# Optimization experiments

Measured on AMD Instinct MI355X. Metric: run time of the kernel, lower is better.

## Reference

```python
import jax, jax.numpy as jnp
import numpy as np

EPS = 1e-5

def conv1x1(x, W, b):
    # x: [B,C,H,W], W: [O,C], b: [O] -- a 1x1 conv is a per-pixel matmul
    return jnp.einsum('bchw,oc->bohw', x, W) + b[None, :, None, None]

def mean_variance_norm(feat):
    # torch .var(dim=2) is unbiased (ddof=1)
    m = feat.mean(axis=(2, 3), keepdims=True)
    v = feat.var(axis=(2, 3), ddof=1, keepdims=True)
    return (feat - m) / jnp.sqrt(v + EPS)

def setup_inputs() -> dict:
    key = jax.random.key(0)
    ks = jax.random.split(key, 10)
    B, C, H, W = 4, 256, 64, 64
    sc = 1.0 / np.sqrt(C)
    return {
        'content': jax.random.normal(ks[0], (B, C, H, W), jnp.float32),
        'style': jax.random.normal(ks[1], (B, C, H, W), jnp.float32),
        'content_key': jax.random.normal(ks[2], (B, C, H, W), jnp.float32),
        'style_key': jax.random.normal(ks[3], (B, C, H, W), jnp.float32),
        'Wf': jax.random.normal(ks[4], (C, C), jnp.float32) * sc,
        'bf': jnp.zeros((C,), jnp.float32),
        'Wg': jax.random.normal(ks[5], (C, C), jnp.float32) * sc,
        'bg': jnp.zeros((C,), jnp.float32),
        'Wh': jax.random.normal(ks[6], (C, C), jnp.float32) * sc,
        'bh': jnp.zeros((C,), jnp.float32),
    }

def reference(content, style, content_key, style_key, Wf, bf, Wg, bg, Wh, bh):
    Fq = conv1x1(content_key, Wf, bf)   # [B,Ck,H,W]
    G = conv1x1(style_key, Wg, bg)      # [B,Ck,Hs,Ws]
    Hv = conv1x1(style, Wh, bh)         # [B,C,Hs,Ws]
    b, _, h, w = Fq.shape
    _, C, hs, ws = Hv.shape
    N, M = h * w, hs * ws
    q = Fq.reshape(b, -1, N).transpose(0, 2, 1)   # [B,N,Ck]
    k = G.reshape(b, -1, M)                        # [B,Ck,M]
    style_flat = Hv.reshape(b, C, M).transpose(0, 2, 1)  # [B,M,C]
    # masks are all-ones -> attn_mask all zeros -> no masking (faithful to None path)
    S = jax.nn.softmax(jnp.einsum('bnc,bcm->bnm', q, k), axis=-1)  # [B,N,M]
    mean = jnp.einsum('bnm,bmc->bnc', S, style_flat)               # [B,N,C]
    std = jnp.sqrt(jax.nn.relu(
        jnp.einsum('bnm,bmc->bnc', S, style_flat * style_flat) - mean * mean))
    mean = mean.reshape(b, h, w, C).transpose(0, 3, 1, 2)  # [B,C,H,W]
    std = std.reshape(b, h, w, C).transpose(0, 3, 1, 2)
    return std * mean_variance_norm(content) + mean
```

## Files before the change

kernel.cpp:

```cpp
#include <hip/hip_runtime.h>


typedef unsigned int u32;
typedef unsigned short u16;
typedef _Float16 f16x8 __attribute__((ext_vector_type(8)));
typedef float f32x4 __attribute__((ext_vector_type(4)));
typedef float f32x16 __attribute__((ext_vector_type(16)));
typedef unsigned int u32x2 __attribute__((ext_vector_type(2)));
typedef unsigned __attribute__((address_space(3))) as3_u32;
typedef const unsigned __attribute__((address_space(1))) as1_u32;

#define L2E 1.44269504088896340736f
#define MFMA(a, b, c) __builtin_amdgcn_mfma_f32_16x16x32_f16(a, b, c, 0, 0, 0)
#define MFMA32(a, b, c) __builtin_amdgcn_mfma_f32_32x32x16_f16(a, b, c, 0, 0, 0)
#define EXP2(x) __builtin_amdgcn_exp2f(x)

__device__ __forceinline__ u16 h_bits(_Float16 h) { return __builtin_bit_cast(u16, h); }
__device__ __forceinline__ u16 f2h(float f) { return h_bits((_Float16)f); }
__device__ __forceinline__ u32 pk2(float a, float b) {
    return (u32)f2h(a) | ((u32)f2h(b) << 16);
}

__device__ __forceinline__ f16x8 ldh8(const u16* p) {
    uint4 v = *(const uint4*)p;
    return __builtin_bit_cast(f16x8, v);
}

__device__ __forceinline__ void gll16(const u16* g, const void* lds) {
    __builtin_amdgcn_global_load_lds((as1_u32*)g,
                                     (as3_u32*)(unsigned)(unsigned long long)lds,
                                     16, 0, 0);
}

__device__ __forceinline__ u32x2 pl32_swap(u32 a, u32 b) {
#if __has_builtin(__builtin_amdgcn_permlane32_swap)
    return __builtin_amdgcn_permlane32_swap(a, b, false, false);
#else
    asm("v_permlane32_swap_b32 %0, %1" : "+v"(a), "+v"(b));
    u32x2 r; r.x = a; r.y = b; return r;
#endif
}

__global__ void k_stats(const float* __restrict__ content,
                        float* __restrict__ cm, float* __restrict__ cr) {
    int blk = blockIdx.x;
    const float* p = content + (size_t)blk * 4096;
    int t = threadIdx.x;
    float s = 0.f, ss = 0.f;
    for (int i = 0; i < 4; i++) {
        float4 v = *(const float4*)(p + (i * 256 + t) * 4);
        s  += (v.x + v.y) + (v.z + v.w);
        ss += (v.x * v.x + v.y * v.y) + (v.z * v.z + v.w * v.w);
    }
    for (int d = 32; d >= 1; d >>= 1) { s += __shfl_xor(s, d); ss += __shfl_xor(ss, d); }
    __shared__ __align__(16) float as[4], ass[4];
    int w = t >> 6;
    if ((t & 63) == 0) { as[w] = s; ass[w] = ss; }
    __syncthreads();
    if (t == 0) {
        s  = (as[0] + as[1]) + (as[2] + as[3]);
        ss = (ass[0] + ass[1]) + (ass[2] + ass[3]);
        float mean = s * (1.0f / 4096.0f);
        float var = (ss - s * mean) * (1.0f / 4095.0f);
        cm[blk] = mean;
        cr[blk] = rsqrtf(var + 1e-5f);
    }
}

__global__ void k_prep(const float* __restrict__ style, const float* __restrict__ ckey,
                       const float* __restrict__ skey,
                       const float* __restrict__ Wf, const float* __restrict__ Wg,
                       const float* __restrict__ Wh,
                       u16* __restrict__ X1, u16* __restrict__ X2, u16* __restrict__ Cc,
                       u16* __restrict__ Wb) {
    int z = blockIdx.z, t = threadIdx.x;
    if (z >= 12) {
        if (blockIdx.y != 0) return;
        int m = z - 12;
        const float* src = (m == 0) ? Wf : ((m == 1) ? Wg : Wh);
        u16* dst = Wb + m * 65536;
        int i = (blockIdx.x * 256 + t) * 4;
        float4 v = *(const float4*)(src + i);
        ushort4 o;
        o.x = f2h(v.x); o.y = f2h(v.y); o.z = f2h(v.z); o.w = f2h(v.w);
        *(ushort4*)(dst + i) = o;
        return;
    }
    int tensor = z >> 2, b = z & 3;
    const float* src = ((tensor == 0) ? style : ((tensor == 1) ? ckey : skey))
                       + (size_t)b * 256 * 4096;
    u16* dst = ((tensor == 0) ? X1 : ((tensor == 1) ? X2 : Cc)) + (size_t)b * 4096 * 256;
    int c0 = blockIdx.y * 64, t0 = blockIdx.x * 64;
    __shared__ __align__(16) float ls[64][65];
    int tr = t >> 4, tc = t & 15;
    for (int i = 0; i < 4; i++) {
        int c_off = i * 16 + tr;
        float4 v = *(const float4*)(src + (size_t)(c0 + c_off) * 4096 + t0 + tc * 4);
        ls[tc * 4 + 0][c_off] = v.x;
        ls[tc * 4 + 1][c_off] = v.y;
        ls[tc * 4 + 2][c_off] = v.z;
        ls[tc * 4 + 3][c_off] = v.w;
    }
    __syncthreads();
    for (int i = 0; i < 4; i++) {
        int tokrow = i * 16 + tr;
        ushort4 o;
        o.x = f2h(ls[tokrow][tc * 4 + 0]);
        o.y = f2h(ls[tokrow][tc * 4 + 1]);
        o.z = f2h(ls[tokrow][tc * 4 + 2]);
        o.w = f2h(ls[tokrow][tc * 4 + 3]);
        *(ushort4*)(dst + (size_t)(t0 + tokrow) * 256 + c0 + tc * 4) = o;
    }
}

__launch_bounds__(256, 2)
__global__ void k_gemm(const u16* X1, const u16* X2, u16* Cc,
                       u16* A, u16* Bv, const u16* __restrict__ Wb,
                       const float* __restrict__ bfp, const float* __restrict__ bgp,
                       const float* __restrict__ bhp) {
    int mode = blockIdx.z, b = blockIdx.y, tok0 = blockIdx.x * 128;
    const u16* X = ((mode == 0) ? X2 : ((mode == 1) ? (const u16*)Cc : X1))
                   + (size_t)b * 4096 * 256;
    const u16* W = Wb + mode * 65536;
    const float* bias = (mode == 0) ? bfp : ((mode == 1) ? bgp : bhp);
    __shared__ __align__(16) u16 wt[256 * 40];
    int t = threadIdx.x, w = t >> 6, lane = t & 63, ln = lane & 15, quad = lane >> 4;

    f32x4 acc[8][4];
    for (int i = 0; i < 8; i++)
        for (int j = 0; j < 4; j++) acc[i][j] = f32x4{0.f, 0.f, 0.f, 0.f};

    for (int ks = 0; ks < 8; ks++) {
        {
            const u16* wr = W + t * 256 + ks * 32;
            uint4 w0 = *(const uint4*)(wr + 0);
            uint4 w1 = *(const uint4*)(wr + 8);
            uint4 w2 = *(const uint4*)(wr + 16);
            uint4 w3 = *(const uint4*)(wr + 24);
            *(uint4*)(wt + t * 40 + 0)  = w0;
            *(uint4*)(wt + t * 40 + 8)  = w1;
            *(uint4*)(wt + t * 40 + 16) = w2;
            *(uint4*)(wt + t * 40 + 24) = w3;
        }
        __syncthreads();
        f16x8 wf[4];
        #pragma unroll
        for (int ct = 0; ct < 4; ct++)
            wf[ct] = ldh8(wt + (w * 64 + ct * 16 + ln) * 40 + quad * 8);
        #pragma unroll
        for (int rt = 0; rt < 8; rt++) {
            f16x8 xf = ldh8(X + (size_t)(tok0 + rt * 16 + ln) * 256 + ks * 32 + quad * 8);
            if (mode < 2) {
                #pragma unroll
                for (int ct = 0; ct < 4; ct++) acc[rt][ct] = MFMA(xf, wf[ct], acc[rt][ct]);
            } else {
                #pragma unroll
                for (int ct = 0; ct < 4; ct++) acc[rt][ct] = MFMA(wf[ct], xf, acc[rt][ct]);
            }
        }
        __syncthreads();
    }

    if (mode < 2) {
        u16* O = ((mode == 0) ? A : Cc) + (size_t)b * 4096 * 256;
        float bv[4];
        #pragma unroll
        for (int ct = 0; ct < 4; ct++) bv[ct] = bias[w * 64 + ct * 16 + ln];
        #pragma unroll
        for (int rt = 0; rt < 8; rt++)
            #pragma unroll
            for (int ct = 0; ct < 4; ct++)
                #pragma unroll
                for (int r = 0; r < 4; r++) {
                    int tok = tok0 + rt * 16 + quad * 4 + r;
                    int o = w * 64 + ct * 16 + ln;
                    O[(size_t)tok * 256 + o] = f2h(acc[rt][ct][r] + bv[ct]);
                }
    } else {
        u16* OV = Bv + (size_t)b * 256 * 4096;
        #pragma unroll
        for (int ct = 0; ct < 4; ct++)
            #pragma unroll
            for (int r = 0; r < 4; r++) {
                int o = w * 64 + ct * 16 + quad * 4 + r;
                float bb = bias[o];
                #pragma unroll
                for (int rt = 0; rt < 8; rt++) {
                    int tok = tok0 + rt * 16 + ln;
                    OV[(size_t)o * 4096 + tok] = f2h(acc[rt][ct][r] + bb);
                }
            }
    }
}

__launch_bounds__(256)
__attribute__((amdgpu_waves_per_eu(2, 2)))
__global__ void k_flash(const u16* __restrict__ Qt, const u16* __restrict__ Kt,
                        const u16* __restrict__ Vt,
                        const float* __restrict__ content, const float* __restrict__ cm,
                        const float* __restrict__ cr, float* __restrict__ out) {
    __shared__ __align__(16) char smem[67584];
    const u16* KsU = (const u16*)smem;
    int t = threadIdx.x, w = t >> 6, l = t & 63, lq = l & 31, h = l >> 5;

    int b = blockIdx.y, q0 = blockIdx.x * 128, coff = blockIdx.z * 64;

    const u16* Kg = Kt + (size_t)b * 4096 * 256;
    const u16* Vg = Vt + ((size_t)b * 256 + coff) * 4096;

    const u16* ksrc;
    {
        int qb = w * 1024 + l * 16;
        int r0 = qb >> 9;
        int swz = (qb & 511) ^ ((r0 & 7) << 4);
        ksrc = Kg + r0 * 256 + (swz >> 1);
    }
    const char* ldsKw = smem + w * 1024;

    int uu = (h ^ (lq & 7)) << 3;
    int tab0 = uu, tab1 = 16 ^ uu, tab2 = 32 ^ uu, tab3 = 48 ^ uu;
    int kb0 = lq * 256;

    f16x8 qf[16];
    {
        const u16* qp = Qt + ((size_t)b * 4096 + q0 + w * 32 + lq) * 256 + h * 8;
        #pragma unroll
        for (int ks = 0; ks < 16; ks++) qf[ks] = ldh8(qp + ks * 16);
    }

    f32x16 am[2], aq[2];
    #pragma unroll
    for (int i = 0; i < 16; i++) { am[0][i] = 0.f; am[1][i] = 0.f; aq[0][i] = 0.f; aq[1][i] = 0.f; }
    float mrow = -1e30f, lrow = 0.f;

    #pragma unroll
    for (int i = 0; i < 8; i++) gll16(ksrc + i * 2048, ldsKw + i * 4096);
    asm volatile("s_waitcnt vmcnt(0)" ::: "memory");
    __builtin_amdgcn_s_barrier();

    int koffB = 0;
    for (int it = 0; it < 64; it++) {
        if (it < 63) {
            int m0n = (it + 1) * 16384;
            #pragma unroll
            for (int i = 0; i < 8; i++)
                gll16(ksrc + m0n + i * 2048, ldsKw + (koffB ^ 32768) + i * 4096);
        }

        int kb = (koffB >> 1) + kb0;
        f32x16 s0, s1;
        #pragma unroll
        for (int i = 0; i < 16; i++) { s0[i] = 0.f; s1[i] = 0.f; }
        __builtin_amdgcn_s_setprio(1);
        #pragma unroll
        for (int ks = 0; ks < 16; ks++) {
            int off = ((ks & 3) == 0 ? tab0 : (ks & 3) == 1 ? tab1
                      : (ks & 3) == 2 ? tab2 : tab3) + (ks >> 2) * 64;
            f16x8 k0 = ldh8(KsU + kb + off);
            s0 = MFMA32(k0, qf[ks], s0);
            f16x8 k1 = ldh8(KsU + kb + 8192 + off);
            s1 = MFMA32(k1, qf[ks], s1);
        }
        __builtin_amdgcn_s_setprio(0);

        const u16* Vit = Vg + it * 64;
        f16x8 vfr[4][2];
        #pragma unroll
        for (int ks = 0; ks < 4; ks++)
            #pragma unroll
            for (int ct = 0; ct < 2; ct++)
                vfr[ks][ct] = ldh8(Vit + (size_t)(ct * 32 + lq) * 4096 + ks * 16 + h * 8);

        float m8[8];
        #pragma unroll
        for (int r = 0; r < 8; r++)
            m8[r] = fmaxf(fmaxf(s0[r], s0[r + 8]), fmaxf(s1[r], s1[r + 8]));
        #pragma unroll
        for (int d = 4; d >= 1; d >>= 1)
            #pragma unroll
            for (int r = 0; r < d; r++) m8[r] = fmaxf(m8[r], m8[r + d]);
        float mt = fmaxf(m8[0], __shfl_xor(m8[0], 32));

        float mn, al;
        bool resc = !__all(mt - mrow <= 8.0f);
        if (resc) {
            mn = fmaxf(mrow, mt);
            al = EXP2((mrow - mn) * L2E);
            mrow = mn;
        } else {
            mn = mrow;
            al = 1.0f;
        }
        float base = mn * L2E;
        #pragma unroll
        for (int r = 0; r < 16; r++) {
            float p0 = (float)(_Float16)EXP2(__builtin_fmaf(s0[r], L2E, -base));
            float p1 = (float)(_Float16)EXP2(__builtin_fmaf(s1[r], L2E, -base));
            s0[r] = p0; s1[r] = p1;
        }
        float a8[8];
        #pragma unroll
        for (int r = 0; r < 8; r++)
            a8[r] = (s0[r] + s0[r + 8]) + (s1[r] + s1[r + 8]);
        #pragma unroll
        for (int d = 4; d >= 1; d >>= 1)
            #pragma unroll
            for (int r = 0; r < d; r++) a8[r] += a8[r + d];
        float rs = a8[0] + __shfl_xor(a8[0], 32);
        lrow = lrow * al + rs;

        if (resc) {
            #pragma unroll
            for (int r = 0; r < 16; r++) {
                float sc = __shfl(al, 8 * (r >> 2) + 4 * h + (r & 3));
                am[0][r] *= sc; am[1][r] *= sc;
                aq[0][r] *= sc; aq[1][r] *= sc;
            }
        }

        f16x8 pfr[4];
        #pragma unroll
        for (int mt2 = 0; mt2 < 2; mt2++) {
            f32x16 sv = mt2 ? s1 : s0;
            u32 d0 = pk2(sv[0], sv[1]),  d1 = pk2(sv[2], sv[3]);
            u32 d2 = pk2(sv[4], sv[5]),  d3 = pk2(sv[6], sv[7]);
            u32 d4 = pk2(sv[8], sv[9]),  d5 = pk2(sv[10], sv[11]);
            u32 d6 = pk2(sv[12], sv[13]), d7 = pk2(sv[14], sv[15]);
            u32x2 p02 = pl32_swap(d0, d2);
            u32x2 p13 = pl32_swap(d1, d3);
            u32x2 p46 = pl32_swap(d4, d6);
            u32x2 p57 = pl32_swap(d5, d7);
            uint4 fa = {p02.x, p13.x, p02.y, p13.y};
            uint4 fb = {p46.x, p57.x, p46.y, p57.y};
            pfr[mt2 * 2 + 0] = __builtin_bit_cast(f16x8, fa);
            pfr[mt2 * 2 + 1] = __builtin_bit_cast(f16x8, fb);
        }

        __builtin_amdgcn_s_setprio(1);
        #pragma unroll
        for (int ks = 0; ks < 4; ks++) {
            f16x8 pf = pfr[ks];
            #pragma unroll
            for (int ct = 0; ct < 2; ct++) {
                f16x8 vf = vfr[ks][ct];
                am[ct] = MFMA32(pf, vf, am[ct]);
                f16x8 vh = vf * vf;
                f16x8 vl = __builtin_elementwise_fma(vf, vf, -vh);
                aq[ct] = MFMA32(pf, vh, aq[ct]);
                aq[ct] = MFMA32(pf, vl, aq[ct]);
            }
        }
        __builtin_amdgcn_s_setprio(0);

        asm volatile("s_waitcnt vmcnt(0)" ::: "memory");
        __builtin_amdgcn_s_barrier();
        koffB ^= 32768;
    }

    float inv = 1.0f / lrow;
    float iv[16];
    #pragma unroll
    for (int r = 0; r < 16; r++) iv[r] = __shfl(inv, (r & 3) + 8 * (r >> 2) + 4 * h);
    float* Ms = (float*)smem;
    float* Ss = (float*)(smem + 33792);
    #pragma unroll
    for (int ct = 0; ct < 2; ct++)
        #pragma unroll
        for (int rq = 0; rq < 4; rq++) {
            f32x4 mv, sv;
            #pragma unroll
            for (int j = 0; j < 4; j++) {
                int r = 4 * rq + j;
                float mean = am[ct][r] * iv[r];
                float ex2 = aq[ct][r] * iv[r];
                float var = ex2 - mean * mean;
                mv[j] = mean;
                sv[j] = sqrtf(fmaxf(var, 0.f));
            }
            int c = ct * 32 + lq;
            int qloc = w * 32 + 8 * rq + 4 * h;
            *(f32x4*)(Ms + c * 132 + qloc) = mv;
            *(f32x4*)(Ss + c * 132 + qloc) = sv;
        }
    __syncthreads();
    #pragma unroll
    for (int pass = 0; pass < 8; pass++) {
        int c = pass * 8 + (t >> 5);
        int qloc = (t & 31) * 4;
        f32x4 mv = *(const f32x4*)(Ms + c * 132 + qloc);
        f32x4 sv = *(const f32x4*)(Ss + c * 132 + qloc);
        int gc = coff + c;
        size_t basei = ((size_t)b * 256 + gc) * 4096 + q0 + qloc;
        float4 cv = *(const float4*)(content + basei);
        float cmv = cm[b * 256 + gc], crv = cr[b * 256 + gc];
        float4 o;
        o.x = sv[0] * ((cv.x - cmv) * crv) + mv[0];
        o.y = sv[1] * ((cv.y - cmv) * crv) + mv[1];
        o.z = sv[2] * ((cv.z - cmv) * crv) + mv[2];
        o.w = sv[3] * ((cv.w - cmv) * crv) + mv[3];
        *(float4*)(out + basei) = o;
    }
}

extern "C" void kernel_launch(void* const* d_in, const int* in_sizes, int n_in,
                              void* d_out, int out_size, void* d_ws, size_t ws_size,
                              hipStream_t stream) {
    const float* content = (const float*)d_in[0];
    const float* style   = (const float*)d_in[1];
    const float* ckey    = (const float*)d_in[2];
    const float* skey    = (const float*)d_in[3];
    const float* Wf      = (const float*)d_in[4];
    const float* bfp     = (const float*)d_in[5];
    const float* Wg      = (const float*)d_in[6];
    const float* bgp     = (const float*)d_in[7];
    const float* Wh      = (const float*)d_in[8];
    const float* bhp     = (const float*)d_in[9];
    float* out = (float*)d_out;
    char* ws = (char*)d_ws;

    float* cm = (float*)(ws + 0);
    float* cr = (float*)(ws + 4096);
    u16*   Wb = (u16*)(ws + 8192);
    u16*   A  = (u16*)(ws + 1048576);
    u16*   Bv = (u16*)(ws + 9437184);
    u16*   Cc = (u16*)(ws + 17825792);
    u16*   X1 = (u16*)d_out;
    u16*   X2 = (u16*)d_out + 4194304;

    k_stats<<<dim3(1024), 256, 0, stream>>>(content, cm, cr);
    k_prep<<<dim3(64, 4, 15), 256, 0, stream>>>(style, ckey, skey, Wf, Wg, Wh,
                                                X1, X2, Cc, Wb);
    k_gemm<<<dim3(32, 4, 3), 256, 0, stream>>>(X1, X2, Cc, A, Bv, Wb, bfp, bgp, bhp);
    k_flash<<<dim3(32, 4, 4), 256, 0, stream>>>(A, Cc, Bv, content, cm, cr, out);
}
```

Baseline: 406.8 us.

## Defer PV MFMAs by one iteration to overlap with softmax

The P·V and P·V² MFMA accumulation is software-pipelined: each iteration keeps its packed probabilities and V fragments in registers, and issues them at the start of the next iteration, alongside the max/sum reductions. A drain step after the loop finishes the last tile. This lets the matrix unit run while the softmax VALU work executes, instead of running serially after it. In exchange, V loads are now waited on at the end-of-iteration vmcnt(0), so they no longer hide behind the QK MFMAs. Register pressure also rises from the held fragments, and the setprio hints around PV are dropped.

```diff
diff --git a/kernel.cpp b/kernel.cpp
--- a/kernel.cpp
+++ b/kernel.cpp
@@ -233,6 +233,15 @@
     for (int i = 0; i < 16; i++) { am[0][i] = 0.f; am[1][i] = 0.f; aq[0][i] = 0.f; aq[1][i] = 0.f; }
     float mrow = -1e30f, lrow = 0.f;
 
+    f16x8 pheld[4];
+    f16x8 vheld[4][2];
+    #pragma unroll
+    for (int i = 0; i < 4; i++) {
+        pheld[i] = f16x8{0, 0, 0, 0, 0, 0, 0, 0};
+        vheld[i][0] = f16x8{0, 0, 0, 0, 0, 0, 0, 0};
+        vheld[i][1] = f16x8{0, 0, 0, 0, 0, 0, 0, 0};
+    }
+
     #pragma unroll
     for (int i = 0; i < 8; i++) gll16(ksrc + i * 2048, ldsKw + i * 4096);
     asm volatile("s_waitcnt vmcnt(0)" ::: "memory");
@@ -263,13 +272,19 @@
         }
         __builtin_amdgcn_s_setprio(0);
 
-        const u16* Vit = Vg + it * 64;
-        f16x8 vfr[4][2];
-        #pragma unroll
-        for (int ks = 0; ks < 4; ks++)
-            #pragma unroll
-            for (int ct = 0; ct < 2; ct++)
-                vfr[ks][ct] = ldh8(Vit + (size_t)(ct * 32 + lq) * 4096 + ks * 16 + h * 8);
+        #pragma unroll
+        for (int ks = 0; ks < 4; ks++) {
+            f16x8 pf = pheld[ks];
+            #pragma unroll
+            for (int ct = 0; ct < 2; ct++) {
+                f16x8 vf = vheld[ks][ct];
+                am[ct] = MFMA32(pf, vf, am[ct]);
+                f16x8 vh = vf * vf;
+                f16x8 vl = __builtin_elementwise_fma(vf, vf, -vh);
+                aq[ct] = MFMA32(pf, vh, aq[ct]);
+                aq[ct] = MFMA32(pf, vl, aq[ct]);
+            }
+        }
 
         float m8[8];
         #pragma unroll
@@ -318,7 +333,6 @@
             }
         }
 
-        f16x8 pfr[4];
         #pragma unroll
         for (int mt2 = 0; mt2 < 2; mt2++) {
             f32x16 sv = mt2 ? s1 : s0;
@@ -332,29 +346,37 @@
             u32x2 p57 = pl32_swap(d5, d7);
             uint4 fa = {p02.x, p13.x, p02.y, p13.y};
             uint4 fb = {p46.x, p57.x, p46.y, p57.y};
-            pfr[mt2 * 2 + 0] = __builtin_bit_cast(f16x8, fa);
-            pfr[mt2 * 2 + 1] = __builtin_bit_cast(f16x8, fb);
-        }
-
-        __builtin_amdgcn_s_setprio(1);
-        #pragma unroll
-        for (int ks = 0; ks < 4; ks++) {
-            f16x8 pf = pfr[ks];
-            #pragma unroll
-            for (int ct = 0; ct < 2; ct++) {
-                f16x8 vf = vfr[ks][ct];
-                am[ct] = MFMA32(pf, vf, am[ct]);
-                f16x8 vh = vf * vf;
-                f16x8 vl = __builtin_elementwise_fma(vf, vf, -vh);
-                aq[ct] = MFMA32(pf, vh, aq[ct]);
-                aq[ct] = MFMA32(pf, vl, aq[ct]);
-            }
-        }
-        __builtin_amdgcn_s_setprio(0);
+            pheld[mt2 * 2 + 0] = __builtin_bit_cast(f16x8, fa);
+            pheld[mt2 * 2 + 1] = __builtin_bit_cast(f16x8, fb);
+        }
+
+        {
+            const u16* Vit = Vg + it * 64;
+            #pragma unroll
+            for (int ks = 0; ks < 4; ks++)
+                #pragma unroll
+                for (int ct = 0; ct < 2; ct++)
+                    vheld[ks][ct] =
+                        ldh8(Vit + (size_t)(ct * 32 + lq) * 4096 + ks * 16 + h * 8);
+        }
 
         asm volatile("s_waitcnt vmcnt(0)" ::: "memory");
         __builtin_amdgcn_s_barrier();
         koffB ^= 32768;
+    }
+
+    #pragma unroll
+    for (int ks = 0; ks < 4; ks++) {
+        f16x8 pf = pheld[ks];
+        #pragma unroll
+        for (int ct = 0; ct < 2; ct++) {
+            f16x8 vf = vheld[ks][ct];
+            am[ct] = MFMA32(pf, vf, am[ct]);
+            f16x8 vh = vf * vf;
+            f16x8 vl = __builtin_elementwise_fma(vf, vf, -vh);
+            aq[ct] = MFMA32(pf, vh, aq[ct]);
+            aq[ct] = MFMA32(pf, vl, aq[ct]);
+        }
     }
 
     float inv = 1.0f / lrow;
```

Result: slower. 419.5 us (+3.1%).

## Split KV tile across wave pairs in flash kernel and merge softmax partials

Applied to the files above, without the earlier changes.

The flash kernel now handles 64 queries per block instead of 128, with the four waves arranged as two query groups times two key halves. Each wave runs its own online softmax over half of every 64-key tile, and the two halves are merged through LDS at the end. The double-buffered K prefetch is replaced by a single buffer that is loaded at the top of each iteration and waited on before use. LDS use drops and the grid doubles, with waves_per_eu raised to 3 so more blocks can be resident, at the cost of exposed K load latency, extra barriers and a final reduction step.

```diff
diff --git a/kernel.cpp b/kernel.cpp
--- a/kernel.cpp
+++ b/kernel.cpp
@@ -194,36 +194,37 @@
 }
 
 __launch_bounds__(256)
-__attribute__((amdgpu_waves_per_eu(2, 2)))
+__attribute__((amdgpu_waves_per_eu(3)))
 __global__ void k_flash(const u16* __restrict__ Qt, const u16* __restrict__ Kt,
                         const u16* __restrict__ Vt,
                         const float* __restrict__ content, const float* __restrict__ cm,
                         const float* __restrict__ cr, float* __restrict__ out) {
-    __shared__ __align__(16) char smem[67584];
+    __shared__ __align__(16) char smem[36864];
     const u16* KsU = (const u16*)smem;
-    int t = threadIdx.x, w = t >> 6, l = t & 63, lq = l & 31, h = l >> 5;
-
-    int b = blockIdx.y, q0 = blockIdx.x * 128, coff = blockIdx.z * 64;
+    int t = threadIdx.x, w4 = t >> 6, l = t & 63, lq = l & 31, h = l >> 5;
+    int qg = w4 & 1, mh = w4 >> 1;
+
+    int b = blockIdx.y, q0 = blockIdx.x * 64, coff = blockIdx.z * 64;
 
     const u16* Kg = Kt + (size_t)b * 4096 * 256;
-    const u16* Vg = Vt + ((size_t)b * 256 + coff) * 4096;
+    const u16* Vg = Vt + ((size_t)b * 256 + coff) * 4096 + mh * 32;
 
     const u16* ksrc;
     {
-        int qb = w * 1024 + l * 16;
+        int qb = w4 * 1024 + l * 16;
         int r0 = qb >> 9;
         int swz = (qb & 511) ^ ((r0 & 7) << 4);
         ksrc = Kg + r0 * 256 + (swz >> 1);
     }
-    const char* ldsKw = smem + w * 1024;
+    const char* ldsKw = smem + w4 * 1024;
 
     int uu = (h ^ (lq & 7)) << 3;
     int tab0 = uu, tab1 = 16 ^ uu, tab2 = 32 ^ uu, tab3 = 48 ^ uu;
-    int kb0 = lq * 256;
+    int kb0 = (mh * 32 + lq) * 256;
 
     f16x8 qf[16];
     {
-        const u16* qp = Qt + ((size_t)b * 4096 + q0 + w * 32 + lq) * 256 + h * 8;
+        const u16* qp = Qt + ((size_t)b * 4096 + q0 + qg * 32 + lq) * 256 + h * 8;
         #pragma unroll
         for (int ks = 0; ks < 16; ks++) qf[ks] = ldh8(qp + ks * 16);
     }
@@ -233,48 +234,51 @@
     for (int i = 0; i < 16; i++) { am[0][i] = 0.f; am[1][i] = 0.f; aq[0][i] = 0.f; aq[1][i] = 0.f; }
     float mrow = -1e30f, lrow = 0.f;
 
-    #pragma unroll
-    for (int i = 0; i < 8; i++) gll16(ksrc + i * 2048, ldsKw + i * 4096);
-    asm volatile("s_waitcnt vmcnt(0)" ::: "memory");
-    __builtin_amdgcn_s_barrier();
-
-    int koffB = 0;
     for (int it = 0; it < 64; it++) {
-        if (it < 63) {
-            int m0n = (it + 1) * 16384;
+        {
+            int m0 = it * 16384;
             #pragma unroll
             for (int i = 0; i < 8; i++)
-                gll16(ksrc + m0n + i * 2048, ldsKw + (koffB ^ 32768) + i * 4096);
-        }
-
-        int kb = (koffB >> 1) + kb0;
-        f32x16 s0, s1;
-        #pragma unroll
-        for (int i = 0; i < 16; i++) { s0[i] = 0.f; s1[i] = 0.f; }
+                gll16(ksrc + m0 + i * 2048, ldsKw + i * 4096);
+        }
+        asm volatile("" ::: "memory");
+        f16x8 vfr[2][2];
+        {
+            const u16* Vit = Vg + it * 64;
+            #pragma unroll
+            for (int ks = 0; ks < 2; ks++)
+                #pragma unroll
+                for (int ct = 0; ct < 2; ct++)
+                    vfr[ks][ct] = ldh8(Vit + (size_t)(ct * 32 + lq) * 4096 + ks * 16 + h * 8);
+        }
+        asm volatile("s_waitcnt vmcnt(4)" ::: "memory");
+        __builtin_amdgcn_s_barrier();
+        asm volatile("" ::: "memory");
+
+        f32x16 sA, sB;
+        #pragma unroll
+        for (int i = 0; i < 16; i++) { sA[i] = 0.f; sB[i] = 0.f; }
         __builtin_amdgcn_s_setprio(1);
         #pragma unroll
-        for (int ks = 0; ks < 16; ks++) {
+        for (int ks = 0; ks < 8; ks++) {
             int off = ((ks & 3) == 0 ? tab0 : (ks & 3) == 1 ? tab1
                       : (ks & 3) == 2 ? tab2 : tab3) + (ks >> 2) * 64;
-            f16x8 k0 = ldh8(KsU + kb + off);
-            s0 = MFMA32(k0, qf[ks], s0);
-            f16x8 k1 = ldh8(KsU + kb + 8192 + off);
-            s1 = MFMA32(k1, qf[ks], s1);
+            sA = MFMA32(ldh8(KsU + kb0 + off), qf[ks], sA);
+        }
+        #pragma unroll
+        for (int ks = 8; ks < 16; ks++) {
+            int off = ((ks & 3) == 0 ? tab0 : (ks & 3) == 1 ? tab1
+                      : (ks & 3) == 2 ? tab2 : tab3) + (ks >> 2) * 64;
+            sB = MFMA32(ldh8(KsU + kb0 + off), qf[ks], sB);
         }
         __builtin_amdgcn_s_setprio(0);
-
-        const u16* Vit = Vg + it * 64;
-        f16x8 vfr[4][2];
-        #pragma unroll
-        for (int ks = 0; ks < 4; ks++)
-            #pragma unroll
-            for (int ct = 0; ct < 2; ct++)
-                vfr[ks][ct] = ldh8(Vit + (size_t)(ct * 32 + lq) * 4096 + ks * 16 + h * 8);
+        f32x16 s;
+        #pragma unroll
+        for (int i = 0; i < 16; i++) s[i] = sA[i] + sB[i];
 
         float m8[8];
         #pragma unroll
-        for (int r = 0; r < 8; r++)
-            m8[r] = fmaxf(fmaxf(s0[r], s0[r + 8]), fmaxf(s1[r], s1[r + 8]));
+        for (int r = 0; r < 8; r++) m8[r] = fmaxf(s[r], s[r + 8]);
         #pragma unroll
         for (int d = 4; d >= 1; d >>= 1)
             #pragma unroll
@@ -293,15 +297,11 @@
         }
         float base = mn * L2E;
         #pragma unroll
-        for (int r = 0; r < 16; r++) {
-            float p0 = (float)(_Float16)EXP2(__builtin_fmaf(s0[r], L2E, -base));
-            float p1 = (float)(_Float16)EXP2(__builtin_fmaf(s1[r], L2E, -base));
-            s0[r] = p0; s1[r] = p1;
-        }
+        for (int r = 0; r < 16; r++)
+            s[r] = (float)(_Float16)EXP2(__builtin_fmaf(s[r], L2E, -base));
         float a8[8];
         #pragma unroll
-        for (int r = 0; r < 8; r++)
-            a8[r] = (s0[r] + s0[r + 8]) + (s1[r] + s1[r + 8]);
+        for (int r = 0; r < 8; r++) a8[r] = s[r] + s[r + 8];
         #pragma unroll
         for (int d = 4; d >= 1; d >>= 1)
             #pragma unroll
@@ -318,27 +318,25 @@
             }
         }
 
-        f16x8 pfr[4];
-        #pragma unroll
-        for (int mt2 = 0; mt2 < 2; mt2++) {
-            f32x16 sv = mt2 ? s1 : s0;
-            u32 d0 = pk2(sv[0], sv[1]),  d1 = pk2(sv[2], sv[3]);
-            u32 d2 = pk2(sv[4], sv[5]),  d3 = pk2(sv[6], sv[7]);
-            u32 d4 = pk2(sv[8], sv[9]),  d5 = pk2(sv[10], sv[11]);
-            u32 d6 = pk2(sv[12], sv[13]), d7 = pk2(sv[14], sv[15]);
+        f16x8 pfr[2];
+        {
+            u32 d0 = pk2(s[0], s[1]),   d1 = pk2(s[2], s[3]);
+            u32 d2 = pk2(s[4], s[5]),   d3 = pk2(s[6], s[7]);
+            u32 d4 = pk2(s[8], s[9]),   d5 = pk2(s[10], s[11]);
+            u32 d6 = pk2(s[12], s[13]), d7 = pk2(s[14], s[15]);
             u32x2 p02 = pl32_swap(d0, d2);
             u32x2 p13 = pl32_swap(d1, d3);
             u32x2 p46 = pl32_swap(d4, d6);
             u32x2 p57 = pl32_swap(d5, d7);
             uint4 fa = {p02.x, p13.x, p02.y, p13.y};
             uint4 fb = {p46.x, p57.x, p46.y, p57.y};
-            pfr[mt2 * 2 + 0] = __builtin_bit_cast(f16x8, fa);
-            pfr[mt2 * 2 + 1] = __builtin_bit_cast(f16x8, fb);
+            pfr[0] = __builtin_bit_cast(f16x8, fa);
+            pfr[1] = __builtin_bit_cast(f16x8, fb);
         }
 
         __builtin_amdgcn_s_setprio(1);
         #pragma unroll
-        for (int ks = 0; ks < 4; ks++) {
+        for (int ks = 0; ks < 2; ks++) {
             f16x8 pf = pfr[ks];
             #pragma unroll
             for (int ct = 0; ct < 2; ct++) {
@@ -352,43 +350,98 @@
         }
         __builtin_amdgcn_s_setprio(0);
 
-        asm volatile("s_waitcnt vmcnt(0)" ::: "memory");
+        asm volatile("" ::: "memory");
         __builtin_amdgcn_s_barrier();
-        koffB ^= 32768;
-    }
-
-    float inv = 1.0f / lrow;
+        asm volatile("" ::: "memory");
+    }
+
+    float* Lsm = (float*)(smem + 16384);
+    __syncthreads();
+    if (h == 0) {
+        Lsm[w4 * 32 + lq] = lrow;
+        Lsm[128 + w4 * 32 + lq] = mrow;
+    }
+    __syncthreads();
+    float lP = Lsm[((mh ^ 1) * 2 + qg) * 32 + lq];
+    float mP = Lsm[128 + ((mh ^ 1) * 2 + qg) * 32 + lq];
+    float M = fmaxf(mrow, mP);
+    float scOwn = EXP2((mrow - M) * L2E);
+    float lC = lrow * scOwn + lP * EXP2((mP - M) * L2E);
+    {
+        #pragma unroll
+        for (int r = 0; r < 16; r++) {
+            float sc = __shfl(scOwn, 8 * (r >> 2) + 4 * h + (r & 3));
+            am[0][r] *= sc; am[1][r] *= sc;
+            aq[0][r] *= sc; aq[1][r] *= sc;
+        }
+    }
+    float* P1 = (float*)smem;
+    #pragma unroll
+    for (int ct = 0; ct < 2; ct++) {
+        __syncthreads();
+        if (mh == 1) {
+            #pragma unroll
+            for (int rq = 0; rq < 4; rq++) {
+                int o = qg * 1024 + lq * 32 + 8 * rq + 4 * h;
+                f32x4 va = {am[ct][4 * rq], am[ct][4 * rq + 1],
+                            am[ct][4 * rq + 2], am[ct][4 * rq + 3]};
+                f32x4 vq = {aq[ct][4 * rq], aq[ct][4 * rq + 1],
+                            aq[ct][4 * rq + 2], aq[ct][4 * rq + 3]};
+                *(f32x4*)(P1 + o) = va;
+                *(f32x4*)(P1 + 2048 + o) = vq;
+            }
+        }
+        __syncthreads();
+        if (mh == 0) {
+            #pragma unroll
+            for (int rq = 0; rq < 4; rq++) {
+                int o = qg * 1024 + lq * 32 + 8 * rq + 4 * h;
+                f32x4 va = *(const f32x4*)(P1 + o);
+                f32x4 vq = *(const f32x4*)(P1 + 2048 + o);
+                #pragma unroll
+                for (int j = 0; j < 4; j++) {
+                    am[ct][4 * rq + j] += va[j];
+                    aq[ct][4 * rq + j] += vq[j];
+                }
+            }
+        }
+    }
+    __syncthreads();
+
+    float inv = 1.0f / lC;
     float iv[16];
     #pragma unroll
     for (int r = 0; r < 16; r++) iv[r] = __shfl(inv, (r & 3) + 8 * (r >> 2) + 4 * h);
     float* Ms = (float*)smem;
-    float* Ss = (float*)(smem + 33792);
+    float* Ss = (float*)(smem + 17408);
+    if (mh == 0) {
+        #pragma unroll
+        for (int ct = 0; ct < 2; ct++)
+            #pragma unroll
+            for (int rq = 0; rq < 4; rq++) {
+                f32x4 mv, sv;
+                #pragma unroll
+                for (int j = 0; j < 4; j++) {
+                    int r = 4 * rq + j;
+                    float mean = am[ct][r] * iv[r];
+                    float ex2 = aq[ct][r] * iv[r];
+                    float var = ex2 - mean * mean;
+                    mv[j] = mean;
+                    sv[j] = sqrtf(fmaxf(var, 0.f));
+                }
+                int c = ct * 32 + lq;
+                int qloc = qg * 32 + 8 * rq + 4 * h;
+                *(f32x4*)(Ms + c * 68 + qloc) = mv;
+                *(f32x4*)(Ss + c * 68 + qloc) = sv;
+            }
+    }
+    __syncthreads();
     #pragma unroll
-    for (int ct = 0; ct < 2; ct++)
-        #pragma unroll
-        for (int rq = 0; rq < 4; rq++) {
-            f32x4 mv, sv;
-            #pragma unroll
-            for (int j = 0; j < 4; j++) {
-                int r = 4 * rq + j;
-                float mean = am[ct][r] * iv[r];
-                float ex2 = aq[ct][r] * iv[r];
-                float var = ex2 - mean * mean;
-                mv[j] = mean;
-                sv[j] = sqrtf(fmaxf(var, 0.f));
-            }
-            int c = ct * 32 + lq;
-            int qloc = w * 32 + 8 * rq + 4 * h;
-            *(f32x4*)(Ms + c * 132 + qloc) = mv;
-            *(f32x4*)(Ss + c * 132 + qloc) = sv;
-        }
-    __syncthreads();
-    #pragma unroll
-    for (int pass = 0; pass < 8; pass++) {
-        int c = pass * 8 + (t >> 5);
-        int qloc = (t & 31) * 4;
-        f32x4 mv = *(const f32x4*)(Ms + c * 132 + qloc);
-        f32x4 sv = *(const f32x4*)(Ss + c * 132 + qloc);
+    for (int pass = 0; pass < 4; pass++) {
+        int c = pass * 16 + (t >> 4);
+        int qloc = (t & 15) * 4;
+        f32x4 mv = *(const f32x4*)(Ms + c * 68 + qloc);
+        f32x4 sv = *(const f32x4*)(Ss + c * 68 + qloc);
         int gc = coff + c;
         size_t basei = ((size_t)b * 256 + gc) * 4096 + q0 + qloc;
         float4 cv = *(const float4*)(content + basei);
@@ -431,5 +484,5 @@
     k_prep<<<dim3(64, 4, 15), 256, 0, stream>>>(style, ckey, skey, Wf, Wg, Wh,
                                                 X1, X2, Cc, Wb);
     k_gemm<<<dim3(32, 4, 3), 256, 0, stream>>>(X1, X2, Cc, A, Bv, Wb, bfp, bgp, bhp);
-    k_flash<<<dim3(32, 4, 4), 256, 0, stream>>>(A, Cc, Bv, content, cm, cr, out);
-}
+    k_flash<<<dim3(64, 4, 4), 256, 0, stream>>>(A, Cc, Bv, content, cm, cr, out);
+}
```

After: 787.4 us. 1.94x slower.

## Halve flash K tile to 32 keys and shrink LDS for higher occupancy

Applied to the files above, without the earlier changes.

Each loop iteration of the flash-attention kernel now processes 32 keys instead of 64, so it runs twice as many iterations with half the K staging buffer and half the score registers. The epilogue writes mean and std through LDS in two 32-channel passes, so total shared memory drops to about 33 KB. The waves-per-EU hint changes from exactly 2 to at least 3, aiming for more resident blocks per CU to hide latency. The cost is twice as many barriers, max/sum reductions and prefetch rounds per key, plus smaller MFMA batches per iteration.

```diff
diff --git a/kernel.cpp b/kernel.cpp
--- a/kernel.cpp
+++ b/kernel.cpp
@@ -194,14 +194,14 @@
 }
 
 __launch_bounds__(256)
-__attribute__((amdgpu_waves_per_eu(2, 2)))
+__attribute__((amdgpu_waves_per_eu(3)))
 __global__ void k_flash(const u16* __restrict__ Qt, const u16* __restrict__ Kt,
                         const u16* __restrict__ Vt,
                         const float* __restrict__ content, const float* __restrict__ cm,
                         const float* __restrict__ cr, float* __restrict__ out) {
-    __shared__ __align__(16) char smem[67584];
+    __shared__ __align__(16) char smem[33792];
     const u16* KsU = (const u16*)smem;
-    int t = threadIdx.x, w = t >> 6, l = t & 63, lq = l & 31, h = l >> 5;
+    int t = threadIdx.x, w4 = t >> 6, l = t & 63, lq = l & 31, h = l >> 5;
 
     int b = blockIdx.y, q0 = blockIdx.x * 128, coff = blockIdx.z * 64;
 
@@ -210,12 +210,12 @@
 
     const u16* ksrc;
     {
-        int qb = w * 1024 + l * 16;
+        int qb = w4 * 1024 + l * 16;
         int r0 = qb >> 9;
         int swz = (qb & 511) ^ ((r0 & 7) << 4);
         ksrc = Kg + r0 * 256 + (swz >> 1);
     }
-    const char* ldsKw = smem + w * 1024;
+    const char* ldsKw = smem + w4 * 1024;
 
     int uu = (h ^ (lq & 7)) << 3;
     int tab0 = uu, tab1 = 16 ^ uu, tab2 = 32 ^ uu, tab3 = 48 ^ uu;
@@ -223,7 +223,7 @@
 
     f16x8 qf[16];
     {
-        const u16* qp = Qt + ((size_t)b * 4096 + q0 + w * 32 + lq) * 256 + h * 8;
+        const u16* qp = Qt + ((size_t)b * 4096 + q0 + w4 * 32 + lq) * 256 + h * 8;
         #pragma unroll
         for (int ks = 0; ks < 16; ks++) qf[ks] = ldh8(qp + ks * 16);
     }
@@ -234,47 +234,43 @@
     float mrow = -1e30f, lrow = 0.f;
 
     #pragma unroll
-    for (int i = 0; i < 8; i++) gll16(ksrc + i * 2048, ldsKw + i * 4096);
+    for (int i = 0; i < 4; i++) gll16(ksrc + i * 2048, ldsKw + i * 4096);
     asm volatile("s_waitcnt vmcnt(0)" ::: "memory");
     __builtin_amdgcn_s_barrier();
 
     int koffB = 0;
-    for (int it = 0; it < 64; it++) {
-        if (it < 63) {
-            int m0n = (it + 1) * 16384;
-            #pragma unroll
-            for (int i = 0; i < 8; i++)
-                gll16(ksrc + m0n + i * 2048, ldsKw + (koffB ^ 32768) + i * 4096);
+    for (int it = 0; it < 128; it++) {
+        if (it < 127) {
+            int m0n = (it + 1) * 8192;
+            #pragma unroll
+            for (int i = 0; i < 4; i++)
+                gll16(ksrc + m0n + i * 2048, ldsKw + (koffB ^ 16384) + i * 4096);
         }
 
         int kb = (koffB >> 1) + kb0;
-        f32x16 s0, s1;
-        #pragma unroll
-        for (int i = 0; i < 16; i++) { s0[i] = 0.f; s1[i] = 0.f; }
+        f32x16 s;
+        #pragma unroll
+        for (int i = 0; i < 16; i++) s[i] = 0.f;
         __builtin_amdgcn_s_setprio(1);
         #pragma unroll
         for (int ks = 0; ks < 16; ks++) {
             int off = ((ks & 3) == 0 ? tab0 : (ks & 3) == 1 ? tab1
                       : (ks & 3) == 2 ? tab2 : tab3) + (ks >> 2) * 64;
-            f16x8 k0 = ldh8(KsU + kb + off);
-            s0 = MFMA32(k0, qf[ks], s0);
-            f16x8 k1 = ldh8(KsU + kb + 8192 + off);
-            s1 = MFMA32(k1, qf[ks], s1);
+            s = MFMA32(ldh8(KsU + kb + off), qf[ks], s);
         }
         __builtin_amdgcn_s_setprio(0);
 
-        const u16* Vit = Vg + it * 64;
-        f16x8 vfr[4][2];
-        #pragma unroll
-        for (int ks = 0; ks < 4; ks++)
+        const u16* Vit = Vg + it * 32;
+        f16x8 vfr[2][2];
+        #pragma unroll
+        for (int ks = 0; ks < 2; ks++)
             #pragma unroll
             for (int ct = 0; ct < 2; ct++)
                 vfr[ks][ct] = ldh8(Vit + (size_t)(ct * 32 + lq) * 4096 + ks * 16 + h * 8);
 
         float m8[8];
         #pragma unroll
-        for (int r = 0; r < 8; r++)
-            m8[r] = fmaxf(fmaxf(s0[r], s0[r + 8]), fmaxf(s1[r], s1[r + 8]));
+        for (int r = 0; r < 8; r++) m8[r] = fmaxf(s[r], s[r + 8]);
         #pragma unroll
         for (int d = 4; d >= 1; d >>= 1)
             #pragma unroll
@@ -293,15 +289,11 @@
         }
         float base = mn * L2E;
         #pragma unroll
-        for (int r = 0; r < 16; r++) {
-            float p0 = (float)(_Float16)EXP2(__builtin_fmaf(s0[r], L2E, -base));
-            float p1 = (float)(_Float16)EXP2(__builtin_fmaf(s1[r], L2E, -base));
-            s0[r] = p0; s1[r] = p1;
-        }
+        for (int r = 0; r < 16; r++)
+            s[r] = (float)(_Float16)EXP2(__builtin_fmaf(s[r], L2E, -base));
         float a8[8];
         #pragma unroll
-        for (int r = 0; r < 8; r++)
-            a8[r] = (s0[r] + s0[r + 8]) + (s1[r] + s1[r + 8]);
+        for (int r = 0; r < 8; r++) a8[r] = s[r] + s[r + 8];
         #pragma unroll
         for (int d = 4; d >= 1; d >>= 1)
             #pragma unroll
@@ -318,27 +310,25 @@
             }
         }
 
-        f16x8 pfr[4];
-        #pragma unroll
-        for (int mt2 = 0; mt2 < 2; mt2++) {
-            f32x16 sv = mt2 ? s1 : s0;
-            u32 d0 = pk2(sv[0], sv[1]),  d1 = pk2(sv[2], sv[3]);
-            u32 d2 = pk2(sv[4], sv[5]),  d3 = pk2(sv[6], sv[7]);
-            u32 d4 = pk2(sv[8], sv[9]),  d5 = pk2(sv[10], sv[11]);
-            u32 d6 = pk2(sv[12], sv[13]), d7 = pk2(sv[14], sv[15]);
+        f16x8 pfr[2];
+        {
+            u32 d0 = pk2(s[0], s[1]),   d1 = pk2(s[2], s[3]);
+            u32 d2 = pk2(s[4], s[5]),   d3 = pk2(s[6], s[7]);
+            u32 d4 = pk2(s[8], s[9]),   d5 = pk2(s[10], s[11]);
+            u32 d6 = pk2(s[12], s[13]), d7 = pk2(s[14], s[15]);
             u32x2 p02 = pl32_swap(d0, d2);
             u32x2 p13 = pl32_swap(d1, d3);
             u32x2 p46 = pl32_swap(d4, d6);
             u32x2 p57 = pl32_swap(d5, d7);
             uint4 fa = {p02.x, p13.x, p02.y, p13.y};
             uint4 fb = {p46.x, p57.x, p46.y, p57.y};
-            pfr[mt2 * 2 + 0] = __builtin_bit_cast(f16x8, fa);
-            pfr[mt2 * 2 + 1] = __builtin_bit_cast(f16x8, fb);
+            pfr[0] = __builtin_bit_cast(f16x8, fa);
+            pfr[1] = __builtin_bit_cast(f16x8, fb);
         }
 
         __builtin_amdgcn_s_setprio(1);
         #pragma unroll
-        for (int ks = 0; ks < 4; ks++) {
+        for (int ks = 0; ks < 2; ks++) {
             f16x8 pf = pfr[ks];
             #pragma unroll
             for (int ct = 0; ct < 2; ct++) {
@@ -354,7 +344,7 @@
 
         asm volatile("s_waitcnt vmcnt(0)" ::: "memory");
         __builtin_amdgcn_s_barrier();
-        koffB ^= 32768;
+        koffB ^= 16384;
     }
 
     float inv = 1.0f / lrow;
@@ -362,9 +352,10 @@
     #pragma unroll
     for (int r = 0; r < 16; r++) iv[r] = __shfl(inv, (r & 3) + 8 * (r >> 2) + 4 * h);
     float* Ms = (float*)smem;
-    float* Ss = (float*)(smem + 33792);
+    float* Ss = (float*)(smem + 16896);
     #pragma unroll
-    for (int ct = 0; ct < 2; ct++)
+    for (int ct = 0; ct < 2; ct++) {
+        __syncthreads();
         #pragma unroll
         for (int rq = 0; rq < 4; rq++) {
             f32x4 mv, sv;
@@ -377,28 +368,28 @@
                 mv[j] = mean;
                 sv[j] = sqrtf(fmaxf(var, 0.f));
             }
-            int c = ct * 32 + lq;
-            int qloc = w * 32 + 8 * rq + 4 * h;
-            *(f32x4*)(Ms + c * 132 + qloc) = mv;
-            *(f32x4*)(Ss + c * 132 + qloc) = sv;
-        }
-    __syncthreads();
-    #pragma unroll
-    for (int pass = 0; pass < 8; pass++) {
-        int c = pass * 8 + (t >> 5);
-        int qloc = (t & 31) * 4;
-        f32x4 mv = *(const f32x4*)(Ms + c * 132 + qloc);
-        f32x4 sv = *(const f32x4*)(Ss + c * 132 + qloc);
-        int gc = coff + c;
-        size_t basei = ((size_t)b * 256 + gc) * 4096 + q0 + qloc;
-        float4 cv = *(const float4*)(content + basei);
-        float cmv = cm[b * 256 + gc], crv = cr[b * 256 + gc];
-        float4 o;
-        o.x = sv[0] * ((cv.x - cmv) * crv) + mv[0];
-        o.y = sv[1] * ((cv.y - cmv) * crv) + mv[1];
-        o.z = sv[2] * ((cv.z - cmv) * crv) + mv[2];
-        o.w = sv[3] * ((cv.w - cmv) * crv) + mv[3];
-        *(float4*)(out + basei) = o;
+            int qloc = w4 * 32 + 8 * rq + 4 * h;
+            *(f32x4*)(Ms + lq * 132 + qloc) = mv;
+            *(f32x4*)(Ss + lq * 132 + qloc) = sv;
+        }
+        __syncthreads();
+        #pragma unroll
+        for (int pass = 0; pass < 4; pass++) {
+            int c = pass * 8 + (t >> 5);
+            int qloc = (t & 31) * 4;
+            f32x4 mv = *(const f32x4*)(Ms + c * 132 + qloc);
+            f32x4 sv = *(const f32x4*)(Ss + c * 132 + qloc);
+            int gc = coff + ct * 32 + c;
+            size_t basei = ((size_t)b * 256 + gc) * 4096 + q0 + qloc;
+            float4 cv = *(const float4*)(content + basei);
+            float cmv = cm[b * 256 + gc], crv = cr[b * 256 + gc];
+            float4 o;
+            o.x = sv[0] * ((cv.x - cmv) * crv) + mv[0];
+            o.y = sv[1] * ((cv.y - cmv) * crv) + mv[1];
+            o.z = sv[2] * ((cv.z - cmv) * crv) + mv[2];
+            o.w = sv[3] * ((cv.w - cmv) * crv) + mv[3];
+            *(float4*)(out + basei) = o;
+        }
     }
 }
 
```

Result: slower. 519.7 us (+27.7%).
